# Kernel optimization log

Measured on AMD Instinct MI355X. Metric: run time of the kernel, lower is better.

Reference implementation:

```python
import jax, jax.numpy as jnp
import numpy as np

N_HEADS = 16

def _apply_rope(x, cos_pos, sin_pos):
    # x: [B,S,H,Dh]; cos_pos/sin_pos: [1,S,1,Dh//2]
    x1, x2 = jnp.split(x, 2, axis=-1)  # matches torch reshape (...,2,Dh//2) split
    x1r = x1 * cos_pos - x2 * sin_pos
    x2r = x2 * cos_pos + x1 * sin_pos
    return jnp.concatenate([x1r, x2r], axis=-1)

def setup_inputs() -> dict:
    key = jax.random.key(0)
    ks = jax.random.split(key, 8)
    B, S, D = 2, 2048, 1024
    Dh = D // N_HEADS
    hidden_states = jax.random.normal(ks[0], (B, S, D), dtype=jnp.float32)
    # rotary tables: cos/sin of theta; use realistic RoPE frequencies
    inv_freq = 1.0 / (10000.0 ** (jnp.arange(0, Dh, 2, dtype=jnp.float32) / Dh))  # [Dh//2]
    t = jnp.arange(S, dtype=jnp.float32)
    freqs = jnp.outer(t, inv_freq)  # [S, Dh//2]
    cos = jnp.cos(freqs)
    sin = jnp.sin(freqs)
    # additive causal mask [1,1,S,S]
    causal = jnp.tril(jnp.ones((S, S), dtype=bool))
    attention_mask = jnp.where(causal, 0.0, -1e9).astype(jnp.float32)[None, None]
    scale = 1.0 / np.sqrt(D)
    Wq = jax.random.normal(ks[1], (D, D), dtype=jnp.float32) * scale
    Wk = jax.random.normal(ks[2], (D, D), dtype=jnp.float32) * scale
    Wv = jax.random.normal(ks[3], (D, D), dtype=jnp.float32) * scale
    Wo = jax.random.normal(ks[4], (D, D), dtype=jnp.float32) * scale
    return {"hidden_states": hidden_states, "cos": cos, "sin": sin,
            "attention_mask": attention_mask, "Wq": Wq, "Wk": Wk, "Wv": Wv, "Wo": Wo}

def reference(hidden_states, cos, sin, attention_mask, Wq, Wk, Wv, Wo):
    B, S, D = hidden_states.shape
    H = N_HEADS
    Dh = D // H
    scaling = Dh ** -0.5
    q = (hidden_states @ Wq).reshape(B, S, H, Dh)
    k = (hidden_states @ Wk).reshape(B, S, H, Dh)
    v = (hidden_states @ Wv).reshape(B, S, H, Dh)
    cos_pos = cos[None, :, None, :]  # [1,S,1,Dh//2]
    sin_pos = sin[None, :, None, :]
    q = _apply_rope(q, cos_pos, sin_pos)
    k = _apply_rope(k, cos_pos, sin_pos)
    # eager attention: [B,H,S,S] scores
    scores = jnp.einsum('bihd,bjhd->bhij', q * scaling, k)
    scores = scores + attention_mask
    probs = jax.nn.softmax(scores, axis=-1)
    out = jnp.einsum('bhij,bjhd->bihd', probs, v).reshape(B, S, D)
    return out @ Wo
```

## Files before the change

kernel.cpp:

```cpp
#include <hip/hip_runtime.h>
#include <cstdint>
#include <cstddef>

using u16 = unsigned short;
using s16x8 = __attribute__((ext_vector_type(8))) short;
using f32x4 = __attribute__((ext_vector_type(4))) float;

#define GADDR(p) ((const __attribute__((address_space(1))) void*)(p))
#define LADDR(p) ((__attribute__((address_space(3))) void*)(p))

static constexpr int S_LEN = 2048;
static constexpr float L2E = 1.44269504088896f;

#if __has_builtin(__builtin_amdgcn_exp2f)
#define EXP2(x) __builtin_amdgcn_exp2f(x)
#else
#define EXP2(x) exp2f(x)
#endif

__device__ __forceinline__ u16 f2bf(float x) {
  union { float f; unsigned u; } v; v.f = x;
  return (u16)((v.u + 0x7FFFu + ((v.u >> 16) & 1u)) >> 16);
}
__device__ __forceinline__ float bf2f(u16 x) {
  union { unsigned u; float f; } v; v.u = (unsigned)x << 16;
  return v.f;
}
__device__ __forceinline__ unsigned pk2(float a, float b) {
#if __has_builtin(__builtin_amdgcn_perm)
  return __builtin_amdgcn_perm(__float_as_uint(b) + 0x8000u,
                               __float_as_uint(a) + 0x8000u, 0x07060302u);
#else
  union { float f; unsigned u; } x, y; x.f = a; y.f = b;
  return ((x.u + 0x8000u) >> 16) | ((y.u + 0x8000u) & 0xFFFF0000u);
#endif
}

__device__ __constant__ unsigned char T_IT[48] = {
  31,31,30,30,29,28,15,14,
  29,28,27,27,26,26,25,24,13,12,
  25,24,23,23,22,22,21,20,11,10,
  21,20,19,19,18,18,17,16,9,8,
  17,16,7,6,
  5,4, 3,2, 1,0};
__device__ __constant__ unsigned char T_C0[48] = {
  0,1,0,1,0,0,0,0,
  1,1,0,1,0,1,0,0,0,0,
  1,1,0,1,0,1,0,0,0,0,
  1,1,0,1,0,1,0,0,0,0,
  1,1,0,0,
  0,0, 0,0, 0,0};

__global__ __launch_bounds__(256) void prep_k(const float* __restrict__ X,
                                              u16* __restrict__ Xb,
                                              const float* __restrict__ Wq,
                                              const float* __restrict__ Wk,
                                              const float* __restrict__ Wv,
                                              const float* __restrict__ Wo,
                                              u16* __restrict__ WtAll) {
  const int bid = blockIdx.x, tid = threadIdx.x;
  if (bid < 4096) {
    int i = (bid * 256 + tid) * 4;
    float4 v = *(const float4*)(X + i);
    uint2 pk; pk.x = pk2(v.x, v.y); pk.y = pk2(v.z, v.w);
    *(uint2*)(Xb + i) = pk;
    return;
  }
  const int r4 = bid - 4096;
  const int z = r4 >> 8, rem = r4 & 255;
  const float* W = (z == 0) ? Wq : (z == 1) ? Wk : (z == 2) ? Wv : Wo;
  u16* Wt = WtAll + ((size_t)z << 20);
  const int k0 = (rem >> 4) * 64, n0 = (rem & 15) * 64;
  __shared__ float t[64][65];
  #pragma unroll
  for (int it = 0; it < 4; ++it) {
    int slot = it * 256 + tid;
    int r = slot >> 4, cq = slot & 15;
    float4 v = *(const float4*)&W[(size_t)(k0 + r) * 1024 + n0 + cq * 4];
    t[r][cq * 4 + 0] = v.x; t[r][cq * 4 + 1] = v.y;
    t[r][cq * 4 + 2] = v.z; t[r][cq * 4 + 3] = v.w;
  }
  __syncthreads();
  #pragma unroll
  for (int it = 0; it < 16; ++it) {
    int slot = it * 256 + tid;
    int rn = slot >> 6, ck = slot & 63;
    Wt[(size_t)(n0 + rn) * 1024 + k0 + ck] = f2bf(t[ck][rn]);
  }
}

__global__ __launch_bounds__(256, 3) void gemm_k(
    const u16* __restrict__ A, const u16* __restrict__ WtAll,
    const float* __restrict__ cosT, const float* __restrict__ sinT,
    u16* __restrict__ Qb, u16* __restrict__ Kb, u16* __restrict__ Vt,
    int modeBase) {
  const int tid = threadIdx.x, lane = tid & 63, wv = tid >> 6;
  const int mode = modeBase + blockIdx.z;
  const u16* Wp = WtAll + ((size_t)mode << 20);
  const int m0 = blockIdx.x * 128, n0 = blockIdx.y * 128;
  const int wm = (wv >> 1) * 64, wn = (wv & 1) * 64;
  __shared__ __align__(16) u16 As[128 * 64];
  __shared__ __align__(16) u16 Bs[128 * 64];
  f32x4 acc[4][4];
  const f32x4 zf = {0.f, 0.f, 0.f, 0.f};
  #pragma unroll
  for (int i = 0; i < 4; ++i)
    #pragma unroll
    for (int j = 0; j < 4; ++j) acc[i][j] = zf;
  const int q = lane >> 4, l15 = lane & 15;

  for (int k0 = 0; k0 < 1024; k0 += 64) {
    __syncthreads();
    #pragma unroll
    for (int call = 0; call < 4; ++call) {
      int slot = call * 256 + tid;
      int row = slot >> 3, u = (slot & 7) ^ (row & 7);
      __builtin_amdgcn_global_load_lds(
          GADDR(A + (size_t)(m0 + row) * 1024 + k0 + u * 8),
          LADDR(As + (size_t)slot * 8), 16, 0, 0);
      __builtin_amdgcn_global_load_lds(
          GADDR(Wp + (size_t)(n0 + row) * 1024 + k0 + u * 8),
          LADDR(Bs + (size_t)slot * 8), 16, 0, 0);
    }
    __syncthreads();
    s16x8 af[4][2], bfr[4][2];
    #pragma unroll
    for (int mt = 0; mt < 4; ++mt) {
      int r = wm + mt * 16 + l15;
      #pragma unroll
      for (int ks = 0; ks < 2; ++ks)
        af[mt][ks] = *(const s16x8*)(As + r * 64 + (((ks * 4 + q) ^ (r & 7)) << 3));
    }
    #pragma unroll
    for (int nt = 0; nt < 4; ++nt) {
      int r = wn + nt * 16 + l15;
      #pragma unroll
      for (int ks = 0; ks < 2; ++ks)
        bfr[nt][ks] = *(const s16x8*)(Bs + r * 64 + (((ks * 4 + q) ^ (r & 7)) << 3));
    }
    #pragma unroll
    for (int ks = 0; ks < 2; ++ks)
      #pragma unroll
      for (int mt = 0; mt < 4; ++mt)
        #pragma unroll
        for (int nt = 0; nt < 4; ++nt)
          acc[mt][nt] = __builtin_amdgcn_mfma_f32_16x16x32_bf16(af[mt][ks], bfr[nt][ks], acc[mt][nt], 0, 0, 0);
  }

  if (mode < 2) {
    u16* outP = (mode == 0) ? Qb : Kb;
    const float scl = (mode == 0) ? 0.125f * L2E : 1.0f;
    #pragma unroll
    for (int mt = 0; mt < 4; ++mt)
      #pragma unroll
      for (int rg = 0; rg < 4; ++rg) {
        int rowg = m0 + wm + mt * 16 + q * 4 + rg;
        int b = rowg >> 11, s = rowg & 2047;
        #pragma unroll
        for (int ntl = 0; ntl < 2; ++ntl) {
          int col = n0 + wn + ntl * 16 + l15;
          int h = col >> 6, dl = col & 31;
          float cc = cosT[s * 32 + dl], ss = sinT[s * 32 + dl];
          float xlo = acc[mt][ntl][rg];
          float xhi = acc[mt][ntl + 2][rg];
          size_t base = ((size_t)(b * 16 + h) * 2048 + s) * 64 + dl;
          outP[base]      = f2bf((xlo * cc - xhi * ss) * scl);
          outP[base + 32] = f2bf((xhi * cc + xlo * ss) * scl);
        }
      }
  } else {
    #pragma unroll
    for (int mt = 0; mt < 4; ++mt) {
      int rowg = m0 + wm + mt * 16 + q * 4;
      int b = rowg >> 11, s = rowg & 2047;
      #pragma unroll
      for (int nt = 0; nt < 4; ++nt) {
        int col = n0 + wn + nt * 16 + l15;
        int h = col >> 6, d = col & 63;
        uint2 pk;
        pk.x = pk2(acc[mt][nt][0], acc[mt][nt][1]);
        pk.y = pk2(acc[mt][nt][2], acc[mt][nt][3]);
        *(uint2*)(Vt + ((size_t)((b * 16 + h) * 64 + d) * 2048 + s)) = pk;
      }
    }
  }
}

__global__ __launch_bounds__(256, 2) void gemmo_k(
    const u16* __restrict__ A, const u16* __restrict__ WtAll,
    float* __restrict__ Of) {
  const int tid = threadIdx.x, lane = tid & 63, wv = tid >> 6;
  const u16* Wp = WtAll + ((size_t)3 << 20);
  const int m0 = blockIdx.x * 64, n0 = blockIdx.y * 128;
  const int wm = (wv >> 1) * 32, wn = (wv & 1) * 64;
  __shared__ __align__(16) u16 As[64 * 64];
  __shared__ __align__(16) u16 Bs[128 * 64];
  f32x4 acc[2][4];
  const f32x4 zf = {0.f, 0.f, 0.f, 0.f};
  #pragma unroll
  for (int i = 0; i < 2; ++i)
    #pragma unroll
    for (int j = 0; j < 4; ++j) acc[i][j] = zf;
  const int q = lane >> 4, l15 = lane & 15;

  for (int k0 = 0; k0 < 1024; k0 += 64) {
    __syncthreads();
    #pragma unroll
    for (int call = 0; call < 2; ++call) {
      int slot = call * 256 + tid;
      int row = slot >> 3, u = (slot & 7) ^ (row & 7);
      __builtin_amdgcn_global_load_lds(
          GADDR(A + (size_t)(m0 + row) * 1024 + k0 + u * 8),
          LADDR(As + (size_t)slot * 8), 16, 0, 0);
    }
    #pragma unroll
    for (int call = 0; call < 4; ++call) {
      int slot = call * 256 + tid;
      int row = slot >> 3, u = (slot & 7) ^ (row & 7);
      __builtin_amdgcn_global_load_lds(
          GADDR(Wp + (size_t)(n0 + row) * 1024 + k0 + u * 8),
          LADDR(Bs + (size_t)slot * 8), 16, 0, 0);
    }
    __syncthreads();
    s16x8 af[2][2], bfr[4][2];
    #pragma unroll
    for (int mt = 0; mt < 2; ++mt) {
      int r = wm + mt * 16 + l15;
      #pragma unroll
      for (int ks = 0; ks < 2; ++ks)
        af[mt][ks] = *(const s16x8*)(As + r * 64 + (((ks * 4 + q) ^ (r & 7)) << 3));
    }
    #pragma unroll
    for (int nt = 0; nt < 4; ++nt) {
      int r = wn + nt * 16 + l15;
      #pragma unroll
      for (int ks = 0; ks < 2; ++ks)
        bfr[nt][ks] = *(const s16x8*)(Bs + r * 64 + (((ks * 4 + q) ^ (r & 7)) << 3));
    }
    #pragma unroll
    for (int ks = 0; ks < 2; ++ks)
      #pragma unroll
      for (int mt = 0; mt < 2; ++mt)
        #pragma unroll
        for (int nt = 0; nt < 4; ++nt)
          acc[mt][nt] = __builtin_amdgcn_mfma_f32_16x16x32_bf16(af[mt][ks], bfr[nt][ks], acc[mt][nt], 0, 0, 0);
  }

  #pragma unroll
  for (int mt = 0; mt < 2; ++mt)
    #pragma unroll
    for (int rg = 0; rg < 4; ++rg) {
      int rowg = m0 + wm + mt * 16 + q * 4 + rg;
      #pragma unroll
      for (int nt = 0; nt < 4; ++nt) {
        int col = n0 + wn + nt * 16 + l15;
        Of[(size_t)rowg * 1024 + col] = acc[mt][nt][rg];
      }
    }
}

__global__ __launch_bounds__(256, 4) void flash_k(
    const u16* __restrict__ Qb, const u16* __restrict__ Kb,
    const u16* __restrict__ Vt, u16* __restrict__ Aout,
    char* __restrict__ Pscr) {
  const int tid = threadIdx.x, lane = tid & 63, wv = tid >> 6;
  const int q = lane >> 4, l15 = lane & 15;
  __shared__ __align__(16) u16 Ks[128 * 64];
  __shared__ __align__(16) u16 Vs[64 * 128];
  u16* Pw = Ks + wv * 2048;
  const f32x4 zf = {0.f, 0.f, 0.f, 0.f};

  const unsigned c = blockIdx.x;
  const int bh = (int)(c & 31u), local = (int)(c >> 5);
  const int it = T_IT[local], c0 = T_C0[local];
  const int len = (it >> 1) + 1, mid = (len + 1) >> 1;
  const int jt0 = c0 ? mid : 0;
  const int jtE = (it >= 16) ? (c0 ? len : mid) : len;
  const int i0 = it * 64;
  const int iw = i0 + wv * 16 + l15;
  const u16* Qh = Qb + (size_t)bh * S_LEN * 64;
  const u16* Kh = Kb + (size_t)bh * S_LEN * 64;
  const u16* Vh = Vt + (size_t)bh * 64 * S_LEN;

  s16x8 bq[2];
  #pragma unroll
  for (int ks = 0; ks < 2; ++ks)
    bq[ks] = *(const s16x8*)(Qh + (size_t)iw * 64 + ks * 32 + q * 8);

  f32x4 O[4];
  float mst = -1e30f, lst = 0.f;
  #pragma unroll
  for (int i = 0; i < 4; ++i) O[i] = zf;

  for (int jt = jt0; jt < jtE; ++jt) {
    const int j0 = jt * 128;
    __syncthreads();
    #pragma unroll
    for (int cc = 0; cc < 4; ++cc) {
      const int wc = cc * 4 + wv;
      {
        int jr = wc * 8 + (lane >> 3);
        int u = (lane & 7) ^ (jr & 7);
        __builtin_amdgcn_global_load_lds(
            GADDR(Kh + (size_t)(j0 + jr) * 64 + u * 8),
            LADDR(Ks + wc * 512), 16, 0, 0);
      }
      {
        int d = wc * 4 + (lane >> 4);
        int uv = (lane & 15) ^ (d & 15);
        __builtin_amdgcn_global_load_lds(
            GADDR(Vh + (size_t)d * S_LEN + j0 + uv * 8),
            LADDR(Vs + wc * 512), 16, 0, 0);
      }
    }
    __syncthreads();

    f32x4 sf[8];
    #pragma unroll
    for (int j = 0; j < 8; ++j) sf[j] = zf;
    #pragma unroll
    for (int ks = 0; ks < 2; ++ks)
      #pragma unroll
      for (int mt = 0; mt < 8; ++mt) {
        int jr = mt * 16 + l15;
        int u = ((ks * 4 + q) ^ (jr & 7));
        s16x8 ak = *(const s16x8*)(Ks + jr * 64 + u * 8);
        sf[mt] = __builtin_amdgcn_mfma_f32_16x16x32_bf16(ak, bq[ks], sf[mt], 0, 0, 0);
      }

    if (jt == len - 1) {
      #pragma unroll
      for (int mt = 0; mt < 8; ++mt)
        #pragma unroll
        for (int rg = 0; rg < 4; ++rg) {
          int j = j0 + mt * 16 + q * 4 + rg;
          if (j > iw) sf[mt][rg] = -1e30f;
        }
    }

    __syncthreads();

    float mx = sf[0][0];
    #pragma unroll
    for (int mt = 0; mt < 8; ++mt)
      #pragma unroll
      for (int rg = 0; rg < 4; ++rg) mx = fmaxf(mx, sf[mt][rg]);
    mx = fmaxf(mx, __shfl_xor(mx, 16, 64));
    mx = fmaxf(mx, __shfl_xor(mx, 32, 64));
    const bool nonew = __all(mx <= mst);
    float al = 1.0f;
    if (!nonew) {
      float mn = fmaxf(mst, mx);
      al = EXP2(mst - mn);
      mst = mn;
    }
    float sum = 0.f;
    #pragma unroll
    for (int mt = 0; mt < 8; ++mt) {
      float p0 = EXP2(sf[mt][0] - mst), p1 = EXP2(sf[mt][1] - mst);
      float p2 = EXP2(sf[mt][2] - mst), p3 = EXP2(sf[mt][3] - mst);
      sum += (p0 + p1) + (p2 + p3);
      uint2 pk; pk.x = pk2(p0, p1); pk.y = pk2(p2, p3);
      int cj = (mt * 4 + q) ^ l15;
      *(uint2*)(Pw + l15 * 128 + cj * 4) = pk;
    }
    sum += __shfl_xor(sum, 16, 64);
    sum += __shfl_xor(sum, 32, 64);
    if (!nonew) {
      lst = al * lst + sum;
      #pragma unroll
      for (int ntd = 0; ntd < 4; ++ntd)
        #pragma unroll
        for (int rg = 0; rg < 4; ++rg) O[ntd][rg] *= al;
    } else {
      lst += sum;
    }

    asm volatile("s_waitcnt lgkmcnt(0)" ::: "memory");

    s16x8 bp[4];
    #pragma unroll
    for (int ks = 0; ks < 4; ++ks) {
      int u0 = ks * 8 + q * 2;
      union { s16x8 v; uint2 d[2]; } f;
      f.d[0] = *(const uint2*)(Pw + l15 * 128 + ((u0) ^ l15) * 4);
      f.d[1] = *(const uint2*)(Pw + l15 * 128 + ((u0 + 1) ^ l15) * 4);
      bp[ks] = f.v;
    }
    #pragma unroll
    for (int ks = 0; ks < 4; ++ks)
      #pragma unroll
      for (int ntd = 0; ntd < 4; ++ntd) {
        int d = ntd * 16 + l15;
        int uv = (ks * 4 + q) ^ l15;
        s16x8 av = *(const s16x8*)(Vs + d * 128 + uv * 8);
        O[ntd] = __builtin_amdgcn_mfma_f32_16x16x32_bf16(av, bp[ks], O[ntd], 0, 0, 0);
      }
  }

  if (it < 16) {
    const float inv = 1.0f / lst;
    const int b = bh >> 4, h = bh & 15;
    u16* dst = Aout + ((size_t)(b * 2048 + iw)) * 1024 + h * 64;
    #pragma unroll
    for (int ntd = 0; ntd < 4; ++ntd) {
      uint2 pk;
      pk.x = pk2(O[ntd][0] * inv, O[ntd][1] * inv);
      pk.y = pk2(O[ntd][2] * inv, O[ntd][3] * inv);
      *(uint2*)(dst + ntd * 16 + q * 4) = pk;
    }
  } else {
    const int slot = (bh * 16 + (it - 16)) * 2 + c0;
    char* pb = Pscr + (size_t)slot * 8704;
    float* Pm = (float*)pb;
    u16* Po = (u16*)(pb + 512);
    const int il = wv * 16 + l15;
    if (q == 0) { Pm[il] = mst; Pm[64 + il] = lst; }
    #pragma unroll
    for (int ntd = 0; ntd < 4; ++ntd) {
      uint2 pk;
      pk.x = pk2(O[ntd][0], O[ntd][1]);
      pk.y = pk2(O[ntd][2], O[ntd][3]);
      *(uint2*)(Po + il * 64 + ntd * 16 + q * 4) = pk;
    }
  }
}

__global__ __launch_bounds__(256) void combine_k(const char* __restrict__ Pscr,
                                                 u16* __restrict__ Aout) {
  const int blk = blockIdx.x;
  const int bh = blk >> 4, itm = blk & 15;
  const char* b0 = Pscr + (size_t)((bh * 16 + itm) * 2 + 0) * 8704;
  const char* b1 = Pscr + (size_t)((bh * 16 + itm) * 2 + 1) * 8704;
  const int t = threadIdx.x;
  const int r = t >> 2, dseg = (t & 3) * 16;
  const float m0 = ((const float*)b0)[r], l0 = ((const float*)b0)[64 + r];
  const float m1 = ((const float*)b1)[r], l1 = ((const float*)b1)[64 + r];
  const float M = fmaxf(m0, m1);
  const float w0 = EXP2(m0 - M), w1 = EXP2(m1 - M);
  const float inv = 1.0f / (w0 * l0 + w1 * l1);
  const u16* O0 = (const u16*)(b0 + 512) + r * 64 + dseg;
  const u16* O1 = (const u16*)(b1 + 512) + r * 64 + dseg;
  unsigned outv[8];
  #pragma unroll
  for (int v8 = 0; v8 < 2; ++v8) {
    s16x8 a = *(const s16x8*)(O0 + v8 * 8);
    s16x8 bb = *(const s16x8*)(O1 + v8 * 8);
    #pragma unroll
    for (int jp = 0; jp < 4; ++jp) {
      float e0 = (w0 * bf2f((u16)a[jp * 2])     + w1 * bf2f((u16)bb[jp * 2]))     * inv;
      float e1 = (w0 * bf2f((u16)a[jp * 2 + 1]) + w1 * bf2f((u16)bb[jp * 2 + 1])) * inv;
      outv[v8 * 4 + jp] = pk2(e0, e1);
    }
  }
  const int b = bh >> 4, h = bh & 15;
  const int s = (itm + 16) * 64 + r;
  u16* dst = Aout + ((size_t)(b * 2048 + s)) * 1024 + h * 64 + dseg;
  *(uint4*)dst = *(const uint4*)outv;
  *(uint4*)(dst + 8) = *(const uint4*)(outv + 4);
}

extern "C" void kernel_launch(void* const* d_in, const int* in_sizes, int n_in,
                              void* d_out, int out_size, void* d_ws, size_t ws_size,
                              hipStream_t stream) {
  const float* X    = (const float*)d_in[0];
  const float* cosT = (const float*)d_in[1];
  const float* sinT = (const float*)d_in[2];
  const float* Wq = (const float*)d_in[4];
  const float* Wk = (const float*)d_in[5];
  const float* Wv = (const float*)d_in[6];
  const float* Wo = (const float*)d_in[7];
  float* Of = (float*)d_out;

  u16* ws  = (u16*)d_ws;
  u16* Xb  = ws;
  u16* Wt  = ws + (4u << 20);
  u16* Qb  = ws + (8u << 20);
  u16* Kb  = ws + (12u << 20);
  u16* Vtb = ws + (20u << 20);
  char* Pscr = (char*)d_out;

  prep_k<<<5120, 256, 0, stream>>>(X, Xb, Wq, Wk, Wv, Wo, Wt);
  gemm_k<<<dim3(32, 8, 3), 256, 0, stream>>>(Xb, Wt, cosT, sinT, Qb, Kb, Vtb, 0);
  flash_k<<<1536, 256, 0, stream>>>(Qb, Kb, Vtb, Xb, Pscr);
  combine_k<<<512, 256, 0, stream>>>(Pscr, Xb);
  gemmo_k<<<dim3(64, 8), 256, 0, stream>>>(Xb, Wt, Of);
}
```

Before: 180.9 us.

## Drop split-KV flash blocks and combine kernel; schedule query tiles by length

Removes the split-KV scheme, in which long query tiles were split across two blocks with partial results merged by a separate combine kernel. Each query tile is now processed whole by one block, with launch order taken from a new 32-entry table that pairs long and short tiles. This eliminates the combine launch and the scratch round-trip, at the cost of fewer blocks (1024 instead of 1536) and a longer critical path for the longest tiles. gemmo_k's launch bound also rises to 3 blocks per SM, which caps register use per thread.

Measured after the change: 185.8 us. +2.7%, slower.

```diff
diff --git a/kernel.cpp b/kernel.cpp
--- a/kernel.cpp
+++ b/kernel.cpp
@@ -21,10 +21,6 @@
 __device__ __forceinline__ u16 f2bf(float x) {
   union { float f; unsigned u; } v; v.f = x;
   return (u16)((v.u + 0x7FFFu + ((v.u >> 16) & 1u)) >> 16);
-}
-__device__ __forceinline__ float bf2f(u16 x) {
-  union { unsigned u; float f; } v; v.u = (unsigned)x << 16;
-  return v.f;
 }
 __device__ __forceinline__ unsigned pk2(float a, float b) {
 #if __has_builtin(__builtin_amdgcn_perm)
@@ -36,20 +32,11 @@
 #endif
 }
 
-__device__ __constant__ unsigned char T_IT[48] = {
-  31,31,30,30,29,28,15,14,
-  29,28,27,27,26,26,25,24,13,12,
-  25,24,23,23,22,22,21,20,11,10,
-  21,20,19,19,18,18,17,16,9,8,
-  17,16,7,6,
-  5,4, 3,2, 1,0};
-__device__ __constant__ unsigned char T_C0[48] = {
-  0,1,0,1,0,0,0,0,
-  1,1,0,1,0,1,0,0,0,0,
-  1,1,0,1,0,1,0,0,0,0,
-  1,1,0,1,0,1,0,0,0,0,
-  1,1,0,0,
-  0,0, 0,0, 0,0};
+__device__ __constant__ unsigned char T2[32] = {
+  31,30,29,28,27,26,25,24,
+  16,17,18,19,20,21,22,23,
+  15,14,13,12,11,10, 9, 8,
+   0, 1, 2, 3, 4, 5, 6, 7};
 
 __global__ __launch_bounds__(256) void prep_k(const float* __restrict__ X,
                                               u16* __restrict__ Xb,
@@ -186,7 +173,7 @@
   }
 }
 
-__global__ __launch_bounds__(256, 2) void gemmo_k(
+__global__ __launch_bounds__(256, 3) void gemmo_k(
     const u16* __restrict__ A, const u16* __restrict__ WtAll,
     float* __restrict__ Of) {
   const int tid = threadIdx.x, lane = tid & 63, wv = tid >> 6;
@@ -261,8 +248,7 @@
 
 __global__ __launch_bounds__(256, 4) void flash_k(
     const u16* __restrict__ Qb, const u16* __restrict__ Kb,
-    const u16* __restrict__ Vt, u16* __restrict__ Aout,
-    char* __restrict__ Pscr) {
+    const u16* __restrict__ Vt, u16* __restrict__ Aout) {
   const int tid = threadIdx.x, lane = tid & 63, wv = tid >> 6;
   const int q = lane >> 4, l15 = lane & 15;
   __shared__ __align__(16) u16 Ks[128 * 64];
@@ -272,10 +258,8 @@
 
   const unsigned c = blockIdx.x;
   const int bh = (int)(c & 31u), local = (int)(c >> 5);
-  const int it = T_IT[local], c0 = T_C0[local];
-  const int len = (it >> 1) + 1, mid = (len + 1) >> 1;
-  const int jt0 = c0 ? mid : 0;
-  const int jtE = (it >= 16) ? (c0 ? len : mid) : len;
+  const int it = T2[local];
+  const int len = (it >> 1) + 1;
   const int i0 = it * 64;
   const int iw = i0 + wv * 16 + l15;
   const u16* Qh = Qb + (size_t)bh * S_LEN * 64;
@@ -292,7 +276,7 @@
   #pragma unroll
   for (int i = 0; i < 4; ++i) O[i] = zf;
 
-  for (int jt = jt0; jt < jtE; ++jt) {
+  for (int jt = 0; jt < len; ++jt) {
     const int j0 = jt * 128;
     __syncthreads();
     #pragma unroll
@@ -398,66 +382,16 @@
       }
   }
 
-  if (it < 16) {
-    const float inv = 1.0f / lst;
-    const int b = bh >> 4, h = bh & 15;
-    u16* dst = Aout + ((size_t)(b * 2048 + iw)) * 1024 + h * 64;
-    #pragma unroll
-    for (int ntd = 0; ntd < 4; ++ntd) {
-      uint2 pk;
-      pk.x = pk2(O[ntd][0] * inv, O[ntd][1] * inv);
-      pk.y = pk2(O[ntd][2] * inv, O[ntd][3] * inv);
-      *(uint2*)(dst + ntd * 16 + q * 4) = pk;
-    }
-  } else {
-    const int slot = (bh * 16 + (it - 16)) * 2 + c0;
-    char* pb = Pscr + (size_t)slot * 8704;
-    float* Pm = (float*)pb;
-    u16* Po = (u16*)(pb + 512);
-    const int il = wv * 16 + l15;
-    if (q == 0) { Pm[il] = mst; Pm[64 + il] = lst; }
-    #pragma unroll
-    for (int ntd = 0; ntd < 4; ++ntd) {
-      uint2 pk;
-      pk.x = pk2(O[ntd][0], O[ntd][1]);
-      pk.y = pk2(O[ntd][2], O[ntd][3]);
-      *(uint2*)(Po + il * 64 + ntd * 16 + q * 4) = pk;
-    }
-  }
-}
-
-__global__ __launch_bounds__(256) void combine_k(const char* __restrict__ Pscr,
-                                                 u16* __restrict__ Aout) {
-  const int blk = blockIdx.x;
-  const int bh = blk >> 4, itm = blk & 15;
-  const char* b0 = Pscr + (size_t)((bh * 16 + itm) * 2 + 0) * 8704;
-  const char* b1 = Pscr + (size_t)((bh * 16 + itm) * 2 + 1) * 8704;
-  const int t = threadIdx.x;
-  const int r = t >> 2, dseg = (t & 3) * 16;
-  const float m0 = ((const float*)b0)[r], l0 = ((const float*)b0)[64 + r];
-  const float m1 = ((const float*)b1)[r], l1 = ((const float*)b1)[64 + r];
-  const float M = fmaxf(m0, m1);
-  const float w0 = EXP2(m0 - M), w1 = EXP2(m1 - M);
-  const float inv = 1.0f / (w0 * l0 + w1 * l1);
-  const u16* O0 = (const u16*)(b0 + 512) + r * 64 + dseg;
-  const u16* O1 = (const u16*)(b1 + 512) + r * 64 + dseg;
-  unsigned outv[8];
-  #pragma unroll
-  for (int v8 = 0; v8 < 2; ++v8) {
-    s16x8 a = *(const s16x8*)(O0 + v8 * 8);
-    s16x8 bb = *(const s16x8*)(O1 + v8 * 8);
-    #pragma unroll
-    for (int jp = 0; jp < 4; ++jp) {
-      float e0 = (w0 * bf2f((u16)a[jp * 2])     + w1 * bf2f((u16)bb[jp * 2]))     * inv;
-      float e1 = (w0 * bf2f((u16)a[jp * 2 + 1]) + w1 * bf2f((u16)bb[jp * 2 + 1])) * inv;
-      outv[v8 * 4 + jp] = pk2(e0, e1);
-    }
-  }
+  const float inv = 1.0f / lst;
   const int b = bh >> 4, h = bh & 15;
-  const int s = (itm + 16) * 64 + r;
-  u16* dst = Aout + ((size_t)(b * 2048 + s)) * 1024 + h * 64 + dseg;
-  *(uint4*)dst = *(const uint4*)outv;
-  *(uint4*)(dst + 8) = *(const uint4*)(outv + 4);
+  u16* dst = Aout + ((size_t)(b * 2048 + iw)) * 1024 + h * 64;
+  #pragma unroll
+  for (int ntd = 0; ntd < 4; ++ntd) {
+    uint2 pk;
+    pk.x = pk2(O[ntd][0] * inv, O[ntd][1] * inv);
+    pk.y = pk2(O[ntd][2] * inv, O[ntd][3] * inv);
+    *(uint2*)(dst + ntd * 16 + q * 4) = pk;
+  }
 }
 
 extern "C" void kernel_launch(void* const* d_in, const int* in_sizes, int n_in,
@@ -478,11 +412,9 @@
   u16* Qb  = ws + (8u << 20);
   u16* Kb  = ws + (12u << 20);
   u16* Vtb = ws + (20u << 20);
-  char* Pscr = (char*)d_out;
 
   prep_k<<<5120, 256, 0, stream>>>(X, Xb, Wq, Wk, Wv, Wo, Wt);
   gemm_k<<<dim3(32, 8, 3), 256, 0, stream>>>(Xb, Wt, cosT, sinT, Qb, Kb, Vtb, 0);
-  flash_k<<<1536, 256, 0, stream>>>(Qb, Kb, Vtb, Xb, Pscr);
-  combine_k<<<512, 256, 0, stream>>>(Pscr, Xb);
+  flash_k<<<1024, 256, 0, stream>>>(Qb, Kb, Vtb, Xb);
   gemmo_k<<<dim3(64, 8), 256, 0, stream>>>(Xb, Wt, Of);
 }
```

## Fuse split-KV combine into flash kernel via atomic last-arriver flags

Applied to the files above, without the earlier changes.

Removes the separate combine kernel launch. Each split flash block writes its partial result, then increments a per-unit atomic counter, and the second block to arrive merges both partials and writes the final attention rows. The flags are zeroed by the first block of the QKV GEMM kernel. The change also raises the gemmo_k occupancy hint from 2 to 3. This saves one launch and its scheduling gap, at the cost of fences and atomics plus a serialized merge at the tail of some blocks.

Result: slower. 281.4 us (+55.5%).

```diff
diff --git a/kernel.cpp b/kernel.cpp
--- a/kernel.cpp
+++ b/kernel.cpp
@@ -93,8 +93,11 @@
     const u16* __restrict__ A, const u16* __restrict__ WtAll,
     const float* __restrict__ cosT, const float* __restrict__ sinT,
     u16* __restrict__ Qb, u16* __restrict__ Kb, u16* __restrict__ Vt,
-    int modeBase) {
+    unsigned* __restrict__ flags, int modeBase) {
   const int tid = threadIdx.x, lane = tid & 63, wv = tid >> 6;
+  if (blockIdx.x == 0 && blockIdx.y == 0 && blockIdx.z == 0) {
+    flags[tid] = 0u; flags[tid + 256] = 0u;
+  }
   const int mode = modeBase + blockIdx.z;
   const u16* Wp = WtAll + ((size_t)mode << 20);
   const int m0 = blockIdx.x * 128, n0 = blockIdx.y * 128;
@@ -186,7 +189,7 @@
   }
 }
 
-__global__ __launch_bounds__(256, 2) void gemmo_k(
+__global__ __launch_bounds__(256, 3) void gemmo_k(
     const u16* __restrict__ A, const u16* __restrict__ WtAll,
     float* __restrict__ Of) {
   const int tid = threadIdx.x, lane = tid & 63, wv = tid >> 6;
@@ -262,11 +265,12 @@
 __global__ __launch_bounds__(256, 4) void flash_k(
     const u16* __restrict__ Qb, const u16* __restrict__ Kb,
     const u16* __restrict__ Vt, u16* __restrict__ Aout,
-    char* __restrict__ Pscr) {
+    char* __restrict__ Pscr, unsigned* __restrict__ flags) {
   const int tid = threadIdx.x, lane = tid & 63, wv = tid >> 6;
   const int q = lane >> 4, l15 = lane & 15;
   __shared__ __align__(16) u16 Ks[128 * 64];
   __shared__ __align__(16) u16 Vs[64 * 128];
+  __shared__ unsigned s_old;
   u16* Pw = Ks + wv * 2048;
   const f32x4 zf = {0.f, 0.f, 0.f, 0.f};
 
@@ -398,9 +402,9 @@
       }
   }
 
+  const int b = bh >> 4, h = bh & 15;
   if (it < 16) {
     const float inv = 1.0f / lst;
-    const int b = bh >> 4, h = bh & 15;
     u16* dst = Aout + ((size_t)(b * 2048 + iw)) * 1024 + h * 64;
     #pragma unroll
     for (int ntd = 0; ntd < 4; ++ntd) {
@@ -409,9 +413,12 @@
       pk.y = pk2(O[ntd][2] * inv, O[ntd][3] * inv);
       *(uint2*)(dst + ntd * 16 + q * 4) = pk;
     }
-  } else {
-    const int slot = (bh * 16 + (it - 16)) * 2 + c0;
-    char* pb = Pscr + (size_t)slot * 8704;
+    return;
+  }
+
+  const int unit = bh * 16 + (it - 16);
+  {
+    char* pb = Pscr + (size_t)(unit * 2 + c0) * 8704;
     float* Pm = (float*)pb;
     u16* Po = (u16*)(pb + 512);
     const int il = wv * 16 + l15;
@@ -424,40 +431,43 @@
       *(uint2*)(Po + il * 64 + ntd * 16 + q * 4) = pk;
     }
   }
-}
-
-__global__ __launch_bounds__(256) void combine_k(const char* __restrict__ Pscr,
-                                                 u16* __restrict__ Aout) {
-  const int blk = blockIdx.x;
-  const int bh = blk >> 4, itm = blk & 15;
-  const char* b0 = Pscr + (size_t)((bh * 16 + itm) * 2 + 0) * 8704;
-  const char* b1 = Pscr + (size_t)((bh * 16 + itm) * 2 + 1) * 8704;
-  const int t = threadIdx.x;
-  const int r = t >> 2, dseg = (t & 3) * 16;
-  const float m0 = ((const float*)b0)[r], l0 = ((const float*)b0)[64 + r];
-  const float m1 = ((const float*)b1)[r], l1 = ((const float*)b1)[64 + r];
-  const float M = fmaxf(m0, m1);
-  const float w0 = EXP2(m0 - M), w1 = EXP2(m1 - M);
-  const float inv = 1.0f / (w0 * l0 + w1 * l1);
-  const u16* O0 = (const u16*)(b0 + 512) + r * 64 + dseg;
-  const u16* O1 = (const u16*)(b1 + 512) + r * 64 + dseg;
-  unsigned outv[8];
-  #pragma unroll
-  for (int v8 = 0; v8 < 2; ++v8) {
-    s16x8 a = *(const s16x8*)(O0 + v8 * 8);
-    s16x8 bb = *(const s16x8*)(O1 + v8 * 8);
-    #pragma unroll
-    for (int jp = 0; jp < 4; ++jp) {
-      float e0 = (w0 * bf2f((u16)a[jp * 2])     + w1 * bf2f((u16)bb[jp * 2]))     * inv;
-      float e1 = (w0 * bf2f((u16)a[jp * 2 + 1]) + w1 * bf2f((u16)bb[jp * 2 + 1])) * inv;
-      outv[v8 * 4 + jp] = pk2(e0, e1);
-    }
-  }
-  const int b = bh >> 4, h = bh & 15;
-  const int s = (itm + 16) * 64 + r;
-  u16* dst = Aout + ((size_t)(b * 2048 + s)) * 1024 + h * 64 + dseg;
-  *(uint4*)dst = *(const uint4*)outv;
-  *(uint4*)(dst + 8) = *(const uint4*)(outv + 4);
+  __syncthreads();
+  if (tid == 0) {
+    __threadfence();
+    s_old = atomicAdd(&flags[unit], 1u);
+  }
+  __syncthreads();
+  if (s_old != 1u) return;
+  __threadfence();
+
+  {
+    const char* b0p = Pscr + (size_t)(unit * 2 + 0) * 8704;
+    const char* b1p = Pscr + (size_t)(unit * 2 + 1) * 8704;
+    const int r = tid >> 2, dseg = (tid & 3) * 16;
+    const float m0 = ((const float*)b0p)[r], l0 = ((const float*)b0p)[64 + r];
+    const float m1 = ((const float*)b1p)[r], l1 = ((const float*)b1p)[64 + r];
+    const float M = fmaxf(m0, m1);
+    const float w0 = EXP2(m0 - M), w1 = EXP2(m1 - M);
+    const float inv = 1.0f / (w0 * l0 + w1 * l1);
+    const u16* O0 = (const u16*)(b0p + 512) + r * 64 + dseg;
+    const u16* O1 = (const u16*)(b1p + 512) + r * 64 + dseg;
+    unsigned outv[8];
+    #pragma unroll
+    for (int v8 = 0; v8 < 2; ++v8) {
+      s16x8 a = *(const s16x8*)(O0 + v8 * 8);
+      s16x8 bb = *(const s16x8*)(O1 + v8 * 8);
+      #pragma unroll
+      for (int jp = 0; jp < 4; ++jp) {
+        float e0 = (w0 * bf2f((u16)a[jp * 2])     + w1 * bf2f((u16)bb[jp * 2]))     * inv;
+        float e1 = (w0 * bf2f((u16)a[jp * 2 + 1]) + w1 * bf2f((u16)bb[jp * 2 + 1])) * inv;
+        outv[v8 * 4 + jp] = pk2(e0, e1);
+      }
+    }
+    const int s = i0 + r;
+    u16* dst = Aout + ((size_t)(b * 2048 + s)) * 1024 + h * 64 + dseg;
+    *(uint4*)dst = *(const uint4*)outv;
+    *(uint4*)(dst + 8) = *(const uint4*)(outv + 4);
+  }
 }
 
 extern "C" void kernel_launch(void* const* d_in, const int* in_sizes, int n_in,
@@ -477,12 +487,12 @@
   u16* Wt  = ws + (4u << 20);
   u16* Qb  = ws + (8u << 20);
   u16* Kb  = ws + (12u << 20);
+  unsigned* flags = (unsigned*)(ws + (16u << 20));
   u16* Vtb = ws + (20u << 20);
   char* Pscr = (char*)d_out;
 
   prep_k<<<5120, 256, 0, stream>>>(X, Xb, Wq, Wk, Wv, Wo, Wt);
-  gemm_k<<<dim3(32, 8, 3), 256, 0, stream>>>(Xb, Wt, cosT, sinT, Qb, Kb, Vtb, 0);
-  flash_k<<<1536, 256, 0, stream>>>(Qb, Kb, Vtb, Xb, Pscr);
-  combine_k<<<512, 256, 0, stream>>>(Pscr, Xb);
+  gemm_k<<<dim3(32, 8, 3), 256, 0, stream>>>(Xb, Wt, cosT, sinT, Qb, Kb, Vtb, flags, 0);
+  flash_k<<<1536, 256, 0, stream>>>(Qb, Kb, Vtb, Xb, Pscr, flags);
   gemmo_k<<<dim3(64, 8), 256, 0, stream>>>(Xb, Wt, Of);
 }
```
